# Performance work log

Measured on AMD Instinct MI355X. Metric: run time of the kernel, lower is better.

The kernel has to match this reference:

```python
import jax, jax.numpy as jnp
import numpy as np

NUM_HEADS = 8
HEAD_DIM = 32  # token_dim 256 / 8 heads


def setup_inputs() -> dict:
    key = jax.random.key(0)
    ks = jax.random.split(key, 12)
    Q, N, E, D, G = 8192, 65536, 262144, 256, 64
    query_tokens = jax.random.normal(ks[0], (Q, D), dtype=jnp.float32)
    support_feats = jax.random.normal(ks[1], (N, D), dtype=jnp.float32)
    geo_embed = jax.random.normal(ks[2], (Q, G), dtype=jnp.float32)
    q_idx = jnp.sort(jax.random.randint(ks[3], (E,), 0, Q, dtype=jnp.int32)).astype(jnp.int32)
    s_idx = jax.random.randint(ks[4], (E,), 0, N, dtype=jnp.int32)
    # fan-in scaled weights (nn.Linear-like init scale)
    Wq = jax.random.normal(ks[5], (D, D), dtype=jnp.float32) / np.sqrt(D)
    Wk = jax.random.normal(ks[6], (D, D), dtype=jnp.float32) / np.sqrt(D)
    Wv = jax.random.normal(ks[7], (D, D), dtype=jnp.float32) / np.sqrt(D)
    Wg = jax.random.normal(ks[8], (G, D), dtype=jnp.float32) / np.sqrt(G)
    Wo = jax.random.normal(ks[9], (D, D), dtype=jnp.float32) / np.sqrt(D)
    bo = jnp.zeros((D,), dtype=jnp.float32)
    log_tau = jnp.zeros((), dtype=jnp.float32)  # tau = 1.0
    return {"query_tokens": query_tokens, "support_feats": support_feats,
            "geo_embed": geo_embed, "q_idx": q_idx, "s_idx": s_idx,
            "num_queries": Q, "Wq": Wq, "Wk": Wk, "Wv": Wv, "Wg": Wg,
            "Wo": Wo, "bo": bo, "log_tau": log_tau}


def reference(query_tokens, support_feats, geo_embed, q_idx, s_idx, num_queries,
              Wq, Wk, Wv, Wg, Wo, bo, log_tau):
    H, Dh = NUM_HEADS, HEAD_DIM
    E = q_idx.shape[0]
    # dense projections on node features (done once per node, then gathered)
    Qf = query_tokens @ Wq            # [Q, D]
    Kf = support_feats @ Wk           # [N, D]
    Vf = support_feats @ Wv           # [N, D]
    Gf = geo_embed @ Wg               # [Q, D]
    q = Qf[q_idx].reshape(E, H, Dh)
    k = Kf[s_idx].reshape(E, H, Dh)
    v = Vf[s_idx].reshape(E, H, Dh)
    g = Gf[q_idx].reshape(E, H, Dh)
    tau = jnp.exp(log_tau)
    scores = jnp.sum(q * k, axis=-1) / (jnp.sqrt(jnp.float32(Dh)) * tau)  # [E, H]
    # segment softmax over ragged neighbor lists; torch scatter_reduce(amax)
    # starts from zeros with include_self=True -> max with 0
    smax = jnp.maximum(jax.ops.segment_max(scores, q_idx, num_segments=num_queries), 0.0)
    ex = jnp.exp(scores - smax[q_idx])
    ssum = jax.ops.segment_sum(ex, q_idx, num_segments=num_queries)
    alpha = ex / jnp.maximum(ssum[q_idx], 1e-8)                            # [E, H]
    weighted = alpha[..., None] * (v + g)                                  # [E, H, Dh]
    out = jax.ops.segment_sum(weighted, q_idx, num_segments=num_queries)   # [Q, H, Dh]
    out = out.reshape(num_queries, H * Dh)
    return out @ Wo + bo
```

## Files before the change

### kernel.cpp

```cpp
#include <hip/hip_runtime.h>
#include <hip/hip_bf16.h>
#include <hip/hip_fp8.h>

typedef __attribute__((ext_vector_type(8))) short short8v;
typedef __attribute__((ext_vector_type(4))) float f32x4;
typedef __attribute__((ext_vector_type(2))) float f32x2;

#define DEVFN __device__ __forceinline__

DEVFN unsigned short f2bf(float x) {
  __hip_bfloat16 h = __float2bfloat16(x);
  return *reinterpret_cast<unsigned short*>(&h);
}

DEVFN float bf2f(unsigned short u) {
  unsigned int x = ((unsigned int)u) << 16;
  float f;
  __builtin_memcpy(&f, &x, 4);
  return f;
}

DEVFN unsigned char f2fp8(float x) {
  __hip_fp8_e4m3 h(x);
  return *reinterpret_cast<unsigned char*>(&h);
}

#if __has_builtin(__builtin_amdgcn_cvt_pk_f32_fp8)
DEVFN void fp8x4_to_f32(unsigned int u, float* out) {
  f32x2 lo = __builtin_amdgcn_cvt_pk_f32_fp8(u, false);
  f32x2 hi = __builtin_amdgcn_cvt_pk_f32_fp8(u, true);
  out[0] = lo[0]; out[1] = lo[1]; out[2] = hi[0]; out[3] = hi[1];
}
#else
DEVFN float fp8_1_to_f32(unsigned int b) {
  const unsigned int s = (b >> 7) & 1, e = (b >> 3) & 15, m = b & 7;
  unsigned int bits = (s << 31) | ((e + 120) << 23) | (m << 20);
  float f;
  __builtin_memcpy(&f, &bits, 4);
  if (e == 0) f = (s ? -1.f : 1.f) * (float)m * 0.001953125f;
  return f;
}
DEVFN void fp8x4_to_f32(unsigned int u, float* out) {
  out[0] = fp8_1_to_f32(u & 0xff);
  out[1] = fp8_1_to_f32((u >> 8) & 0xff);
  out[2] = fp8_1_to_f32((u >> 16) & 0xff);
  out[3] = fp8_1_to_f32((u >> 24) & 0xff);
}
#endif

DEVFN void gload16(const void* g, void* l) {
  __builtin_amdgcn_global_load_lds(
      (const __attribute__((address_space(1))) void*)g,
      (__attribute__((address_space(3))) void*)l, 16, 0, 0);
}

__global__ __launch_bounds__(256) void prep(
    const float* __restrict__ Wk, const float* __restrict__ Wv,
    const float* __restrict__ Wq, const float* __restrict__ Wo,
    const float* __restrict__ Wg,
    unsigned short* __restrict__ Btkv, unsigned short* __restrict__ Btq,
    unsigned short* __restrict__ Bto, unsigned short* __restrict__ Btg,
    const int* __restrict__ q_idx, int* __restrict__ q_start, int Q, int E) {
  const int b = blockIdx.x, t = threadIdx.x;
  if (b < 256) {
    const int wi = b >> 6, bb = b & 63;
    const float* W = (wi == 0) ? Wk : (wi == 1) ? Wv : (wi == 2) ? Wq : Wo;
    unsigned short* O = (wi == 0) ? Btkv : (wi == 1) ? (Btkv + 65536)
                     : (wi == 2) ? Btq : Bto;
    for (int id = bb * 256 + t; id < 65536; id += 64 * 256) {
      const int n = id >> 8, k = id & 255;
      O[id] = f2bf(W[k * 256 + n]);
    }
  } else if (b < 272) {
    for (int id = (b - 256) * 256 + t; id < 16384; id += 16 * 256) {
      const int n = id >> 6, k = id & 63;
      Btg[id] = f2bf(Wg[k * 256 + n]);
    }
  } else {
    const int q = (b - 272) * 256 + t;
    if (q <= Q) {
      int lo = 0, hi = E;
      while (lo < hi) { int mid = (lo + hi) >> 1; if (q_idx[mid] < q) lo = mid + 1; else hi = mid; }
      q_start[q] = lo;
    }
  }
}

DEVFN void gemm_kv_persist(const float* __restrict__ A,
                           const unsigned short* __restrict__ Bt,
                           unsigned char* __restrict__ KV,
                           int bid, int nwg,
                           unsigned short (*As)[128 * 32],
                           unsigned short (*Bs)[128 * 32]) {
  constexpr int K = 256;
  const int t = threadIdx.x;
  const int wv = t >> 6, l = t & 63;
  const int wr = wv >> 1, wc = wv & 1;
  const int lr = l & 15, lk = l >> 4;

  const int swz = (bid & 7) * (nwg >> 3) + (bid >> 3);
  const int m0 = swz * 128;

  const int wbase = (t & ~63) * 16;
  const int arow = t >> 1, ac0 = (t & 1) * 2;
  const float* Afp = A + (size_t)(m0 + arow) * K + ac0 * 8;

  f32x4 acc[4][4];
#pragma unroll
  for (int m = 0; m < 4; ++m)
#pragma unroll
    for (int n = 0; n < 4; ++n) acc[m][n] = (f32x4){0.f, 0.f, 0.f, 0.f};

  float4 reg0[4], reg1[4];

  auto loadA = [&](float4 (&rg)[4], int k0) {
    const float* p = Afp + k0;
#pragma unroll
    for (int j = 0; j < 4; ++j) rg[j] = *(const float4*)(p + j * 4);
  };
  auto writeA = [&](float4 (&rg)[4], int tile) {
    unsigned short u[16];
#pragma unroll
    for (int j = 0; j < 4; ++j) {
      u[4 * j + 0] = f2bf(rg[j].x); u[4 * j + 1] = f2bf(rg[j].y);
      u[4 * j + 2] = f2bf(rg[j].z); u[4 * j + 3] = f2bf(rg[j].w);
    }
    const int cs0 = ac0 ^ ((arow >> 1) & 3);
    const int cs1 = (ac0 + 1) ^ ((arow >> 1) & 3);
    *(short8v*)&As[tile][arow * 32 + cs0 * 8] = *(short8v*)&u[0];
    *(short8v*)&As[tile][arow * 32 + cs1 * 8] = *(short8v*)&u[8];
  };
  auto loadSlot = [&](int tile) {
    if ((tile & 1) == 0) loadA(reg0, tile * 32);
    else                 loadA(reg1, tile * 32);
  };
  auto writeSlot = [&](int tile) {
    if ((tile & 1) == 0) writeA(reg0, tile);
    else                 writeA(reg1, tile);
  };
  auto stageB = [&](int buf, int p, int k0) {
#pragma unroll
    for (int s = 0; s < 2; ++s) {
      const int cidx = s * 256 + t;
      const int row = cidx >> 2, c = cidx & 3;
      const int cs = c ^ ((row >> 1) & 3);
      gload16(Bt + (size_t)(p * 128 + row) * K + k0 + cs * 8,
              (char*)&Bs[buf][0] + (size_t)s * 4096 + wbase);
    }
  };
  auto compute = [&](int atile, int bbuf) {
    short8v a[4], b[4];
#pragma unroll
    for (int m = 0; m < 4; ++m) {
      const int row = wr * 64 + m * 16 + lr;
      const int cs = lk ^ ((row >> 1) & 3);
      a[m] = *(const short8v*)&As[atile][row * 32 + cs * 8];
    }
#pragma unroll
    for (int n = 0; n < 4; ++n) {
      const int row = wc * 64 + n * 16 + lr;
      const int cs = lk ^ ((row >> 1) & 3);
      b[n] = *(const short8v*)&Bs[bbuf][row * 32 + cs * 8];
    }
#pragma unroll
    for (int m = 0; m < 4; ++m)
#pragma unroll
      for (int n = 0; n < 4; ++n)
        acc[m][n] = __builtin_amdgcn_mfma_f32_16x16x32_bf16(a[m], b[n], acc[m][n], 0, 0, 0);
  };

  stageB(0, 0, 0);
  loadSlot(0);
  loadSlot(1);
  writeSlot(0);
  asm volatile("s_waitcnt lgkmcnt(0)" ::: "memory");
  __builtin_amdgcn_s_barrier();
  __builtin_amdgcn_sched_barrier(0);

#pragma unroll
  for (int i = 0; i < 32; ++i) {
    if (i > 0) {
      __builtin_amdgcn_s_barrier();
      __builtin_amdgcn_sched_barrier(0);
    }
    if (i < 8) {
      if (i + 1 < 8) writeSlot(i + 1);
      stageB((i + 1) & 1, (i + 1) >> 3, ((i + 1) & 7) * 32);
      if (i + 2 < 8) loadSlot(i + 2);
      if (i == 7) asm volatile("s_waitcnt vmcnt(2) lgkmcnt(0)" ::: "memory");
      else        asm volatile("s_waitcnt lgkmcnt(0)" ::: "memory");
    } else {
      if (i + 1 < 32) {
        stageB((i + 1) & 1, (i + 1) >> 3, ((i + 1) & 7) * 32);
        asm volatile("s_waitcnt vmcnt(2)" ::: "memory");
      } else {
        asm volatile("s_waitcnt vmcnt(0)" ::: "memory");
      }
    }
    __builtin_amdgcn_s_barrier();
    __builtin_amdgcn_sched_barrier(0);
    compute(i & 7, i & 1);
    if ((i & 7) == 7) {
      const int p = i >> 3;
#pragma unroll
      for (int m = 0; m < 4; ++m)
#pragma unroll
        for (int n = 0; n < 4; ++n) {
          const f32x4 v = acc[m][n];
          const int col = p * 128 + wc * 64 + n * 16 + lr;
          const int rbase = m0 + wr * 64 + m * 16 + lk * 4;
#pragma unroll
          for (int r = 0; r < 4; ++r)
            KV[(size_t)(rbase + r) * 512 + col] = f2fp8(v[r]);
          acc[m][n] = (f32x4){0.f, 0.f, 0.f, 0.f};
        }
    }
  }
}

template <int KT, bool A_F32, int OUT_MODE, bool HAS_BIAS>
DEVFN void gemm_body(const void* __restrict__ Av,
                     const unsigned short* __restrict__ Bt,
                     void* __restrict__ Cv, const float* __restrict__ bias,
                     int ldc, int bid, int gx, int nwg,
                     unsigned short (*As)[128 * 32],
                     unsigned short (*Bs)[128 * 32]) {
  constexpr int K = KT * 32;

  const int t = threadIdx.x;
  const int wv = t >> 6, l = t & 63;
  const int wr = wv >> 1, wc = wv & 1;
  const int lr = l & 15, lk = l >> 4;

  const int swz = (bid & 7) * (nwg >> 3) + (bid >> 3);
  const int n0 = (swz % gx) * 128;
  const int m0 = (swz / gx) * 128;

  f32x4 acc[4][4];
#pragma unroll
  for (int m = 0; m < 4; ++m)
#pragma unroll
    for (int n = 0; n < 4; ++n) acc[m][n] = (f32x4){0.f, 0.f, 0.f, 0.f};

  const int wbase = (t & ~63) * 16;
  const int arow = t >> 1, ac0 = (t & 1) * 2;
  const float* Afp = A_F32 ? ((const float*)Av + (size_t)(m0 + arow) * K + ac0 * 8)
                           : nullptr;
  float4 reg0[4], reg1[4];

  auto loadA = [&](float4 (&rg)[4], int k0) {
    const float* p = Afp + k0;
#pragma unroll
    for (int j = 0; j < 4; ++j) rg[j] = *(const float4*)(p + j * 4);
  };
  auto writeA = [&](float4 (&rg)[4], int buf) {
    unsigned short u[16];
#pragma unroll
    for (int j = 0; j < 4; ++j) {
      u[4 * j + 0] = f2bf(rg[j].x); u[4 * j + 1] = f2bf(rg[j].y);
      u[4 * j + 2] = f2bf(rg[j].z); u[4 * j + 3] = f2bf(rg[j].w);
    }
    const int cs0 = ac0 ^ ((arow >> 1) & 3);
    const int cs1 = (ac0 + 1) ^ ((arow >> 1) & 3);
    *(short8v*)&As[buf][arow * 32 + cs0 * 8] = *(short8v*)&u[0];
    *(short8v*)&As[buf][arow * 32 + cs1 * 8] = *(short8v*)&u[8];
  };
  auto stageA_lds = [&](int buf, int k0) {
    const unsigned short* Ab = (const unsigned short*)Av;
#pragma unroll
    for (int s = 0; s < 2; ++s) {
      const int cidx = s * 256 + t;
      const int row = cidx >> 2, c = cidx & 3;
      const int cs = c ^ ((row >> 1) & 3);
      gload16(Ab + (size_t)(m0 + row) * K + k0 + cs * 8,
              (char*)&As[buf][0] + (size_t)s * 4096 + wbase);
    }
  };
  auto stageB = [&](int buf, int k0) {
#pragma unroll
    for (int s = 0; s < 2; ++s) {
      const int cidx = s * 256 + t;
      const int row = cidx >> 2, c = cidx & 3;
      const int cs = c ^ ((row >> 1) & 3);
      gload16(Bt + (size_t)(n0 + row) * K + k0 + cs * 8,
              (char*)&Bs[buf][0] + (size_t)s * 4096 + wbase);
    }
  };

  auto compute = [&](int buf) {
    short8v a[4], b[4];
#pragma unroll
    for (int m = 0; m < 4; ++m) {
      const int row = wr * 64 + m * 16 + lr;
      const int cs = lk ^ ((row >> 1) & 3);
      a[m] = *(const short8v*)&As[buf][row * 32 + cs * 8];
    }
#pragma unroll
    for (int n = 0; n < 4; ++n) {
      const int row = wc * 64 + n * 16 + lr;
      const int cs = lk ^ ((row >> 1) & 3);
      b[n] = *(const short8v*)&Bs[buf][row * 32 + cs * 8];
    }
#pragma unroll
    for (int m = 0; m < 4; ++m)
#pragma unroll
      for (int n = 0; n < 4; ++n)
        acc[m][n] = __builtin_amdgcn_mfma_f32_16x16x32_bf16(a[m], b[n], acc[m][n], 0, 0, 0);
  };

  stageB(0, 0);
  if (KT > 1) stageB(1, 32);
  if (A_F32) {
    loadA(reg0, 0);
    if (KT > 1) loadA(reg1, 32);
    writeA(reg0, 0);
  } else {
    stageA_lds(0, 0);
    if (KT > 1) stageA_lds(1, 32);
  }

#pragma unroll
  for (int tt = 0; tt < KT; ++tt) {
    __builtin_amdgcn_s_barrier();
    __builtin_amdgcn_sched_barrier(0);
    if (A_F32) {
      if (tt + 2 < KT) {
        if (((tt + 2) & 1) == 0) loadA(reg0, (tt + 2) * 32);
        else                     loadA(reg1, (tt + 2) * 32);
        stageB((tt + 2) % 3, (tt + 2) * 32);
      }
      if (tt + 1 < KT) {
        if (((tt + 1) & 1) == 0) writeA(reg0, (tt + 1) % 3);
        else                     writeA(reg1, (tt + 1) % 3);
      }
      if (tt < KT - 2)       asm volatile("s_waitcnt vmcnt(8) lgkmcnt(0)" ::: "memory");
      else if (tt == KT - 2) asm volatile("s_waitcnt vmcnt(2) lgkmcnt(0)" ::: "memory");
      else                   asm volatile("s_waitcnt vmcnt(0) lgkmcnt(0)" ::: "memory");
    } else {
      if (tt + 2 < KT) {
        stageA_lds((tt + 2) % 3, (tt + 2) * 32);
        stageB((tt + 2) % 3, (tt + 2) * 32);
      }
      const int rem = (tt + 2 < KT ? tt + 2 : KT - 1) - tt;
      if (rem >= 2)      asm volatile("s_waitcnt vmcnt(8)" ::: "memory");
      else if (rem == 1) asm volatile("s_waitcnt vmcnt(4)" ::: "memory");
      else               asm volatile("s_waitcnt vmcnt(0)" ::: "memory");
    }
    __builtin_amdgcn_s_barrier();
    __builtin_amdgcn_sched_barrier(0);
    compute(tt % 3);
  }

#pragma unroll
  for (int m = 0; m < 4; ++m)
#pragma unroll
    for (int n = 0; n < 4; ++n) {
      const f32x4 v = acc[m][n];
      const int col = n0 + wc * 64 + n * 16 + lr;
      const int rbase = m0 + wr * 64 + m * 16 + lk * 4;
      float bv = 0.f;
      if (HAS_BIAS) bv = bias[col];
#pragma unroll
      for (int r = 0; r < 4; ++r) {
        const float val = v[r] + bv;
        if (OUT_MODE == 0) {
          ((float*)Cv)[(size_t)(rbase + r) * ldc + col] = val;
        } else {
          ((unsigned short*)Cv)[(size_t)(rbase + r) * ldc + col] = f2bf(val);
        }
      }
    }
}

__global__ __launch_bounds__(256) void proj(
    const float* __restrict__ support, const float* __restrict__ query,
    const float* __restrict__ geo,
    const unsigned short* __restrict__ Btkv, const unsigned short* __restrict__ Btq,
    const unsigned short* __restrict__ Btg,
    unsigned char* __restrict__ KV, unsigned short* __restrict__ Qf,
    unsigned short* __restrict__ Gf) {
  __shared__ unsigned short LDSU[40960];
  const int b = blockIdx.x;
  if (b < 512) {
    gemm_kv_persist(support, Btkv, KV, b, 512,
                    (unsigned short (*)[128 * 32])&LDSU[0],
                    (unsigned short (*)[128 * 32])&LDSU[32768]);
  } else if (b < 640) {
    gemm_body<8, true, 1, false>(query, Btq, Qf, nullptr, 256, b - 512, 2, 128,
                                 (unsigned short (*)[128 * 32])&LDSU[0],
                                 (unsigned short (*)[128 * 32])&LDSU[12288]);
  } else {
    gemm_body<2, true, 1, false>(geo, Btg, Gf, nullptr, 256, b - 640, 2, 128,
                                 (unsigned short (*)[128 * 32])&LDSU[0],
                                 (unsigned short (*)[128 * 32])&LDSU[12288]);
  }
}

__global__ __launch_bounds__(256) void gemm_final(
    const unsigned short* __restrict__ A, const unsigned short* __restrict__ Bt,
    void* __restrict__ C, const float* __restrict__ bias) {
  __shared__ unsigned short As[3][128 * 32];
  __shared__ unsigned short Bs[3][128 * 32];
  gemm_body<8, false, 0, true>(A, Bt, C, bias, 256, blockIdx.x, 2, 128, As, Bs);
}

__global__ __launch_bounds__(256) void edge_attn(
    const int* __restrict__ s_idx, const int* __restrict__ q_start,
    const unsigned char* __restrict__ KVb, const unsigned short* __restrict__ Qf,
    const unsigned short* __restrict__ Gf, unsigned short* __restrict__ out_pre,
    const float* __restrict__ log_tau) {
  const int q = blockIdx.x;
  const int t = threadIdx.x;
  const int w = t >> 6;
  const int lane = t & 63;
  const int stream = w * 2 + (lane >> 5);
  const int sl = lane & 31;
  const int start = q_start[q], end = q_start[q + 1];

  const float tau = __expf(log_tau[0]);
  const float rs = 1.0f / (5.656854249492381f * tau);

  float qv[8];
  {
    uint4 qw = *(const uint4*)(Qf + (size_t)q * 256 + sl * 8);
    const unsigned int ws_[4] = {qw.x, qw.y, qw.z, qw.w};
#pragma unroll
    for (int j = 0; j < 4; ++j) {
      qv[2 * j]     = bf2f((unsigned short)(ws_[j] & 0xffffu)) * rs;
      qv[2 * j + 1] = bf2f((unsigned short)(ws_[j] >> 16)) * rs;
    }
  }

  float o[8];
#pragma unroll
  for (int j = 0; j < 8; ++j) o[j] = 0.f;
  float lsum_p = 0.f;

  __shared__ int sseg[1024];

  for (int cb = start; cb < end; cb += 1024) {
    const int nb = min(1024, end - cb);
    __syncthreads();
    for (int jj = t; jj < nb; jj += 256) sseg[jj] = s_idx[cb + jj];
    __syncthreads();

    int j = stream;
    uint2 kc = {}, kn = {}, vc = {}, vn = {};
    if (j < nb) {
      const unsigned char* bp = KVb + (size_t)sseg[j] * 512;
      kc = *(const uint2*)(bp + sl * 8);
      vc = *(const uint2*)(bp + 256 + sl * 8);
    }
    if (j + 8 < nb) {
      const unsigned char* bp = KVb + (size_t)sseg[j + 8] * 512;
      kn = *(const uint2*)(bp + sl * 8);
      vn = *(const uint2*)(bp + 256 + sl * 8);
    }
    while (j < nb) {
      const int j2 = j + 16;
      uint2 k2 = {}, v2 = {};
      if (j2 < nb) {
        const unsigned char* bp = KVb + (size_t)sseg[j2] * 512;
        k2 = *(const uint2*)(bp + sl * 8);
        v2 = *(const uint2*)(bp + 256 + sl * 8);
      }
      float kf[8];
      fp8x4_to_f32(kc.x, kf);
      fp8x4_to_f32(kc.y, kf + 4);
      float p = 0.f;
#pragma unroll
      for (int jj = 0; jj < 8; ++jj) p = fmaf(qv[jj], kf[jj], p);
      p += __shfl_xor(p, 1);
      p += __shfl_xor(p, 2);
      const float ew = __expf(p);
      lsum_p += ew;
      float vf[8];
      fp8x4_to_f32(vc.x, vf);
      fp8x4_to_f32(vc.y, vf + 4);
#pragma unroll
      for (int jj = 0; jj < 8; ++jj) o[jj] = fmaf(ew, vf[jj], o[jj]);
      j += 8;
      kc = kn; vc = vn;
      kn = k2; vn = v2;
    }
  }

  __shared__ float o_sh[8][256];
  __shared__ float l_sh[8][8];
  *(float4*)&o_sh[stream][sl * 8]     = (float4){o[0], o[1], o[2], o[3]};
  *(float4*)&o_sh[stream][sl * 8 + 4] = (float4){o[4], o[5], o[6], o[7]};
  if ((sl & 3) == 0) l_sh[stream][sl >> 2] = lsum_p;
  __syncthreads();

  float osum = 0.f, lsum = 0.f;
  const int h = t >> 5;
#pragma unroll
  for (int s = 0; s < 8; ++s) {
    osum += o_sh[s][t];
    lsum += l_sh[s][h];
  }
  const float inv = 1.0f / fmaxf(lsum, 1e-8f);
  float res = 0.f;
  if (end > start) res = osum * inv + (lsum * inv) * bf2f(Gf[(size_t)q * 256 + t]);
  out_pre[(size_t)q * 256 + t] = f2bf(res);
}

extern "C" void kernel_launch(void* const* d_in, const int* in_sizes, int n_in,
                              void* d_out, int out_size, void* d_ws, size_t ws_size,
                              hipStream_t stream) {
  const float* query   = (const float*)d_in[0];
  const float* support = (const float*)d_in[1];
  const float* geo     = (const float*)d_in[2];
  const int*   q_idx   = (const int*)d_in[3];
  const int*   s_idx   = (const int*)d_in[4];
  const float* Wq      = (const float*)d_in[6];
  const float* Wk      = (const float*)d_in[7];
  const float* Wv      = (const float*)d_in[8];
  const float* Wg      = (const float*)d_in[9];
  const float* Wo      = (const float*)d_in[10];
  const float* bo      = (const float*)d_in[11];
  const float* log_tau = (const float*)d_in[12];

  const int D = 256;
  const int Q = in_sizes[0] / D;
  const int N = in_sizes[1] / D;
  const int E = in_sizes[3];

  unsigned char* wsb = (unsigned char*)d_ws;
  unsigned char*  KV   = wsb;
  unsigned short* Qf   = (unsigned short*)(wsb + (size_t)N * 512);
  unsigned short* Gf   = Qf   + (size_t)Q * 256;
  unsigned short* Opre = Gf   + (size_t)Q * 256;
  unsigned short* Btkv = Opre + (size_t)Q * 256;
  unsigned short* Btq  = Btkv + 512 * 256;
  unsigned short* Btg  = Btq  + 256 * 256;
  unsigned short* Bto  = Btg  + 256 * 64;
  int* q_start = (int*)(Bto + 256 * 256);

  dim3 blk(256);

  prep<<<dim3(305), blk, 0, stream>>>(Wk, Wv, Wq, Wo, Wg,
                                      Btkv, Btq, Bto, Btg, q_idx, q_start, Q, E);

  proj<<<dim3(768), blk, 0, stream>>>(support, query, geo, Btkv, Btq, Btg,
                                      KV, Qf, Gf);

  edge_attn<<<dim3(Q), blk, 0, stream>>>(s_idx, q_start, KV,
                                         Qf, Gf, Opre, log_tau);

  gemm_final<<<dim3(128), blk, 0, stream>>>(Opre, Bto, d_out, bo);
}
```

Before: 76.00 us.

## Load KV weight fragments directly from global memory instead of staging through LDS

The K/V projection kernel now converts the whole 128x256 A tile to bf16 in LDS up front, then streams the B (weight) fragments directly from global memory into registers for each MFMA step. The double-buffered B staging in LDS and the per-step barriers go away, and the proj kernel's LDS allocation shrinks from 80KB to 64KB, which could allow more workgroups per CU. The risk is that the global B loads are exposed latency with no prefetch, though the weights are small (256KB) and likely stay cache-resident.

```diff
diff --git a/kernel.cpp b/kernel.cpp
--- a/kernel.cpp
+++ b/kernel.cpp
@@ -90,8 +90,7 @@
                            const unsigned short* __restrict__ Bt,
                            unsigned char* __restrict__ KV,
                            int bid, int nwg,
-                           unsigned short (*As)[128 * 32],
-                           unsigned short (*Bs)[128 * 32]) {
+                           unsigned short (*As)[128 * 32]) {
   constexpr int K = 256;
   const int t = threadIdx.x;
   const int wv = t >> 6, l = t & 63;
@@ -101,15 +100,8 @@
   const int swz = (bid & 7) * (nwg >> 3) + (bid >> 3);
   const int m0 = swz * 128;
 
-  const int wbase = (t & ~63) * 16;
   const int arow = t >> 1, ac0 = (t & 1) * 2;
   const float* Afp = A + (size_t)(m0 + arow) * K + ac0 * 8;
-
-  f32x4 acc[4][4];
-#pragma unroll
-  for (int m = 0; m < 4; ++m)
-#pragma unroll
-    for (int n = 0; n < 4; ++n) acc[m][n] = (f32x4){0.f, 0.f, 0.f, 0.f};
 
   float4 reg0[4], reg1[4];
 
@@ -138,83 +130,58 @@
     if ((tile & 1) == 0) writeA(reg0, tile);
     else                 writeA(reg1, tile);
   };
-  auto stageB = [&](int buf, int p, int k0) {
-#pragma unroll
-    for (int s = 0; s < 2; ++s) {
-      const int cidx = s * 256 + t;
-      const int row = cidx >> 2, c = cidx & 3;
-      const int cs = c ^ ((row >> 1) & 3);
-      gload16(Bt + (size_t)(p * 128 + row) * K + k0 + cs * 8,
-              (char*)&Bs[buf][0] + (size_t)s * 4096 + wbase);
-    }
-  };
-  auto compute = [&](int atile, int bbuf) {
-    short8v a[4], b[4];
-#pragma unroll
-    for (int m = 0; m < 4; ++m) {
-      const int row = wr * 64 + m * 16 + lr;
-      const int cs = lk ^ ((row >> 1) & 3);
-      a[m] = *(const short8v*)&As[atile][row * 32 + cs * 8];
-    }
-#pragma unroll
-    for (int n = 0; n < 4; ++n) {
-      const int row = wc * 64 + n * 16 + lr;
-      const int cs = lk ^ ((row >> 1) & 3);
-      b[n] = *(const short8v*)&Bs[bbuf][row * 32 + cs * 8];
-    }
-#pragma unroll
-    for (int m = 0; m < 4; ++m)
-#pragma unroll
-      for (int n = 0; n < 4; ++n)
-        acc[m][n] = __builtin_amdgcn_mfma_f32_16x16x32_bf16(a[m], b[n], acc[m][n], 0, 0, 0);
-  };
-
-  stageB(0, 0, 0);
+
   loadSlot(0);
   loadSlot(1);
-  writeSlot(0);
+#pragma unroll
+  for (int tt = 0; tt < 8; ++tt) {
+    writeSlot(tt);
+    if (tt + 2 < 8) loadSlot(tt + 2);
+  }
   asm volatile("s_waitcnt lgkmcnt(0)" ::: "memory");
   __builtin_amdgcn_s_barrier();
   __builtin_amdgcn_sched_barrier(0);
 
-#pragma unroll
-  for (int i = 0; i < 32; ++i) {
-    if (i > 0) {
-      __builtin_amdgcn_s_barrier();
-      __builtin_amdgcn_sched_barrier(0);
-    }
-    if (i < 8) {
-      if (i + 1 < 8) writeSlot(i + 1);
-      stageB((i + 1) & 1, (i + 1) >> 3, ((i + 1) & 7) * 32);
-      if (i + 2 < 8) loadSlot(i + 2);
-      if (i == 7) asm volatile("s_waitcnt vmcnt(2) lgkmcnt(0)" ::: "memory");
-      else        asm volatile("s_waitcnt lgkmcnt(0)" ::: "memory");
-    } else {
-      if (i + 1 < 32) {
-        stageB((i + 1) & 1, (i + 1) >> 3, ((i + 1) & 7) * 32);
-        asm volatile("s_waitcnt vmcnt(2)" ::: "memory");
-      } else {
-        asm volatile("s_waitcnt vmcnt(0)" ::: "memory");
-      }
-    }
-    __builtin_amdgcn_s_barrier();
-    __builtin_amdgcn_sched_barrier(0);
-    compute(i & 7, i & 1);
-    if ((i & 7) == 7) {
-      const int p = i >> 3;
+  f32x4 acc[4][4];
+#pragma unroll
+  for (int m = 0; m < 4; ++m)
+#pragma unroll
+    for (int n = 0; n < 4; ++n) acc[m][n] = (f32x4){0.f, 0.f, 0.f, 0.f};
+
+#pragma unroll
+  for (int p = 0; p < 4; ++p) {
+#pragma unroll
+    for (int i = 0; i < 8; ++i) {
+      short8v b[4];
+#pragma unroll
+      for (int n = 0; n < 4; ++n)
+        b[n] = *(const short8v*)(Bt +
+            (size_t)(p * 128 + wc * 64 + n * 16 + lr) * K + i * 32 + lk * 8);
+      short8v a[4];
+#pragma unroll
+      for (int m = 0; m < 4; ++m) {
+        const int row = wr * 64 + m * 16 + lr;
+        const int cs = lk ^ ((row >> 1) & 3);
+        a[m] = *(const short8v*)&As[i][row * 32 + cs * 8];
+      }
 #pragma unroll
       for (int m = 0; m < 4; ++m)
 #pragma unroll
-        for (int n = 0; n < 4; ++n) {
-          const f32x4 v = acc[m][n];
-          const int col = p * 128 + wc * 64 + n * 16 + lr;
-          const int rbase = m0 + wr * 64 + m * 16 + lk * 4;
-#pragma unroll
-          for (int r = 0; r < 4; ++r)
-            KV[(size_t)(rbase + r) * 512 + col] = f2fp8(v[r]);
-          acc[m][n] = (f32x4){0.f, 0.f, 0.f, 0.f};
-        }
-    }
+        for (int n = 0; n < 4; ++n)
+          acc[m][n] = __builtin_amdgcn_mfma_f32_16x16x32_bf16(a[m], b[n], acc[m][n], 0, 0, 0);
+    }
+#pragma unroll
+    for (int m = 0; m < 4; ++m)
+#pragma unroll
+      for (int n = 0; n < 4; ++n) {
+        const f32x4 v = acc[m][n];
+        const int col = p * 128 + wc * 64 + n * 16 + lr;
+        const int rbase = m0 + wr * 64 + m * 16 + lk * 4;
+#pragma unroll
+        for (int r = 0; r < 4; ++r)
+          KV[(size_t)(rbase + r) * 512 + col] = f2fp8(v[r]);
+        acc[m][n] = (f32x4){0.f, 0.f, 0.f, 0.f};
+      }
   }
 }
 
@@ -379,12 +346,11 @@
     const unsigned short* __restrict__ Btg,
     unsigned char* __restrict__ KV, unsigned short* __restrict__ Qf,
     unsigned short* __restrict__ Gf) {
-  __shared__ unsigned short LDSU[40960];
+  __shared__ unsigned short LDSU[32768];
   const int b = blockIdx.x;
   if (b < 512) {
     gemm_kv_persist(support, Btkv, KV, b, 512,
-                    (unsigned short (*)[128 * 32])&LDSU[0],
-                    (unsigned short (*)[128 * 32])&LDSU[32768]);
+                    (unsigned short (*)[128 * 32])&LDSU[0]);
   } else if (b < 640) {
     gemm_body<8, true, 1, false>(query, Btq, Qf, nullptr, 256, b - 512, 2, 128,
                                  (unsigned short (*)[128 * 32])&LDSU[0],
```

Result: slower. 99.27 us (+30.6%).
